# Kernel tuning notes

Measured on AMD Instinct MI355X. Metric: run time of the kernel, lower is better.

## Reference

```python
import jax, jax.numpy as jnp
import numpy as np

NUM_USERS, NUM_ITEMS = 100000, 50000
N_NODES = NUM_USERS + NUM_ITEMS
N_EDGES = 4_000_000
H = 64
BATCH = 100000
MLP_HIDDEN = 32
N_LAYERS = 3


def setup_inputs() -> dict:
    key = jax.random.key(0)
    ks = jax.random.split(key, 12)
    return {
        "edge_index": jax.random.randint(ks[0], (2, N_EDGES), 0, N_NODES, dtype=jnp.int32),
        "user_ids": jax.random.randint(ks[1], (BATCH,), 0, NUM_USERS, dtype=jnp.int32),
        "item_ids": jax.random.randint(ks[2], (BATCH,), 0, NUM_ITEMS, dtype=jnp.int32),
        "user_emb": jax.random.normal(ks[3], (NUM_USERS, H), jnp.float32),
        "item_emb": jax.random.normal(ks[4], (NUM_ITEMS, H), jnp.float32),
        "Wl": jax.random.normal(ks[5], (N_LAYERS, H, H), jnp.float32) * (1.0 / jnp.sqrt(H)),
        "bl": jnp.zeros((N_LAYERS, H), jnp.float32),
        "Wr": jax.random.normal(ks[6], (N_LAYERS, H, H), jnp.float32) * (1.0 / jnp.sqrt(H)),
        "W1": jax.random.normal(ks[7], (2 * H, MLP_HIDDEN), jnp.float32) * (1.0 / jnp.sqrt(2.0 * H)),
        "b1": jnp.zeros((MLP_HIDDEN,), jnp.float32),
        "W2": jax.random.normal(ks[8], (MLP_HIDDEN, 1), jnp.float32) * (1.0 / jnp.sqrt(1.0 * MLP_HIDDEN)),
        "b2": jnp.zeros((1,), jnp.float32),
    }


def _sage_layer(x, src, dst, Wl_i, bl_i, Wr_i):
    # PyG SAGEConv, mean aggr: out = lin_l(mean_{j in N(i)} x_j) + lin_r(x_i)
    msg = x[src]                                                  # [E, H] gather
    summed = jax.ops.segment_sum(msg, dst, num_segments=N_NODES)  # [N, H] scatter-add
    cnt = jax.ops.segment_sum(jnp.ones((src.shape[0],), x.dtype), dst, num_segments=N_NODES)
    mean = summed / jnp.maximum(cnt, 1.0)[:, None]                # empty neighborhoods -> 0
    return mean @ Wl_i + bl_i + x @ Wr_i


def reference(edge_index, user_ids, item_ids, user_emb, item_emb, Wl, bl, Wr, W1, b1, W2, b2):
    src, dst = edge_index[0], edge_index[1]
    x = jnp.concatenate([user_emb, item_emb], axis=0)  # [N, H]
    for l in range(N_LAYERS):
        x = jax.nn.relu(_sage_layer(x, src, dst, Wl[l], bl[l], Wr[l]))
        # dropout is identity in eval mode
    ue = x[user_ids]                   # [B, H]
    ie = x[item_ids + NUM_USERS]       # [B, H]
    pair = jnp.concatenate([ue, ie], axis=-1)  # [B, 2H]
    h = jax.nn.relu(pair @ W1 + b1)
    rating = (h @ W2 + b2)[:, 0]
    return jnp.clip(rating, 1.0, 5.0)
```

## Files before the change

### kernel.cpp

```cpp
#include <hip/hip_runtime.h>
#include <hip/hip_bf16.h>

#define NUM_USERS 100000
#define NUM_ITEMS 50000
#define N_NODES   150000
#define N_EDGES   4000000
#define H         64
#define BATCH     100000
#define MLP_HIDDEN 32
#define NBUCK     586
#define BCAP      8192

typedef unsigned short ushort_t;

__device__ __forceinline__ float bf2f(ushort_t u) {
    return __uint_as_float(((unsigned)u) << 16);
}
__device__ __forceinline__ ushort_t f2bf(float f) {
    unsigned u = __float_as_uint(f);
    u = u + 0x7FFFu + ((u >> 16) & 1u);
    return (ushort_t)(u >> 16);
}
__device__ __forceinline__ float bfLO(unsigned u) { return __uint_as_float(u << 16); }
__device__ __forceinline__ float bfHI(unsigned u) { return __uint_as_float(u & 0xFFFF0000u); }

__global__ __launch_bounds__(256) void init_kernel(const float* __restrict__ ue,
                                                   const float* __restrict__ ie,
                                                   float* __restrict__ x,
                                                   ushort_t* __restrict__ xh) {
    int i = blockIdx.x * 256 + threadIdx.x;
    const int UN4 = NUM_USERS * H / 4;
    float4 v = (i < UN4) ? ((const float4*)ue)[i] : ((const float4*)ie)[i - UN4];
    ((float4*)x)[i] = v;
    uint2 p;
    p.x = (unsigned)f2bf(v.x) | ((unsigned)f2bf(v.y) << 16);
    p.y = (unsigned)f2bf(v.z) | ((unsigned)f2bf(v.w) << 16);
    ((uint2*)xh)[i] = p;
}

#define SCHUNK 2048
__global__ __launch_bounds__(256) void bucket_scatter_kernel(const int* __restrict__ src,
                                                             const int* __restrict__ dst,
                                                             int* __restrict__ bucketCnt,
                                                             int* __restrict__ ebuf) {
    __shared__ int histL[NBUCK];
    __shared__ int curL[NBUCK];
    int base = blockIdx.x * SCHUNK;
    int end = min(base + SCHUNK, N_EDGES);
    for (int i = threadIdx.x; i < NBUCK; i += 256) histL[i] = 0;
    __syncthreads();
    for (int e = base + threadIdx.x; e < end; e += 256)
        atomicAdd(&histL[dst[e] >> 8], 1);
    __syncthreads();
    for (int b = threadIdx.x; b < NBUCK; b += 256)
        curL[b] = histL[b] ? (b * BCAP + atomicAdd(&bucketCnt[b], histL[b])) : 0;
    __syncthreads();
    for (int e = base + threadIdx.x; e < end; e += 256) {
        int d = dst[e];
        int pos = atomicAdd(&curL[d >> 8], 1);
        ebuf[pos] = (src[e] << 8) | (d & 255);
    }
}

__global__ __launch_bounds__(512) void bucket_build_kernel(const int* __restrict__ ebuf,
                                                           const int* __restrict__ bucketCnt,
                                                           int* __restrict__ deg,
                                                           int* __restrict__ offsets,
                                                           int* __restrict__ csr) {
    __shared__ int degL[256];
    __shared__ int scanL[256];
    __shared__ int curL[256];
    int t = threadIdx.x;
    int b = blockIdx.x;
    int nodeBase = b << 8;
    int start = b * BCAP;
    int cnt = bucketCnt[b];

    if (t < 256) degL[t] = 0;
    __syncthreads();
    for (int i = t; i < cnt; i += 512)
        atomicAdd(&degL[ebuf[start + i] & 255], 1);
    __syncthreads();

    int v = (t < 256) ? degL[t] : 0;
    if (t < 256) scanL[t] = v;
    __syncthreads();
#pragma unroll
    for (int off = 1; off < 256; off <<= 1) {
        int u = (t >= off && t < 256) ? scanL[t - off] : 0;
        __syncthreads();
        if (t < 256) scanL[t] += u;
        __syncthreads();
    }

    if (t < 256) {
        int excl = scanL[t] - v;
        int node = nodeBase + t;
        if (node < N_NODES) {
            deg[node] = v;
            offsets[node] = start + excl;
        }
        curL[t] = excl;
    }
    __syncthreads();

    for (int i = t; i < cnt; i += 512) {
        unsigned p = (unsigned)ebuf[start + i];
        int pos = atomicAdd(&curL[p & 255u], 1);
        csr[start + pos] = (int)(p >> 8);
    }
}

__global__ __launch_bounds__(256, 8) void gather_mean_kernel(const ushort_t* __restrict__ xh,
                                                             ushort_t* __restrict__ mean_bf,
                                                             const int* __restrict__ offsets,
                                                             const int* __restrict__ deg,
                                                             const int* __restrict__ csr) {
    int slot = threadIdx.x >> 6;
    int lane = threadIdx.x & 63;
    int q    = lane >> 4;
    int fp   = lane & 15;
    int node = blockIdx.x * 4 + slot;

    int base = offsets[node];
    int cnt  = deg[node];
    const uint2* xr = (const uint2*)xh;

    float a0 = 0.f, a1 = 0.f, a2 = 0.f, a3 = 0.f;

    for (int c = 0; c < cnt; c += 64) {
        int n = min(64, cnt - c);
        int sid = (c + lane < cnt) ? csr[base + c + lane] : 0;
        int nquad = (n + 3) >> 2;
#define PROC(JJ) { int e = 4 * (JJ) + q;                                  \
        int s = __shfl(sid, e, 64);                                       \
        uint2 u = xr[s * 16 + fp];                                        \
        if (c + e >= cnt) { u.x = 0u; u.y = 0u; }                         \
        a0 += bfLO(u.x); a1 += bfHI(u.x); a2 += bfLO(u.y); a3 += bfHI(u.y); }
        int j = 0;
        for (; j + 2 <= nquad; j += 2) { PROC(j) PROC(j + 1) }
        for (; j < nquad; ++j) { PROC(j) }
#undef PROC
    }

    a0 += __shfl_xor(a0, 16, 64); a1 += __shfl_xor(a1, 16, 64);
    a2 += __shfl_xor(a2, 16, 64); a3 += __shfl_xor(a3, 16, 64);
    a0 += __shfl_xor(a0, 32, 64); a1 += __shfl_xor(a1, 32, 64);
    a2 += __shfl_xor(a2, 32, 64); a3 += __shfl_xor(a3, 32, 64);

    if (lane < 16) {
        float rc = 1.0f / fmaxf((float)cnt, 1.0f);
        uint2 p;
        p.x = (unsigned)f2bf(a0 * rc) | ((unsigned)f2bf(a1 * rc) << 16);
        p.y = (unsigned)f2bf(a2 * rc) | ((unsigned)f2bf(a3 * rc) << 16);
        *(uint2*)&mean_bf[node * H + fp * 4] = p;
    }
}

__global__ __launch_bounds__(256) void transform_kernel(float* __restrict__ x,
                                                        ushort_t* __restrict__ xh,
                                                        const ushort_t* __restrict__ mean_bf,
                                                        const float* __restrict__ Wl,
                                                        const float* __restrict__ bl,
                                                        const float* __restrict__ Wr,
                                                        int writeBf) {
    __shared__ float    sWl[H * H];
    __shared__ float    sWr[H * H];
    __shared__ unsigned sMT[H / 2][128];
    __shared__ unsigned sXT[H / 2][128];

    int t = threadIdx.x;
    int node0 = blockIdx.x * 128;

    for (int i = t; i < H * H / 4; i += 256) {
        ((float4*)sWl)[i] = ((const float4*)Wl)[i];
        ((float4*)sWr)[i] = ((const float4*)Wr)[i];
    }
#pragma unroll
    for (int it = 0; it < 8; ++it) {
        int idx = it * 256 + t;
        int n = idx & 127;
        int qd = idx >> 7;
        int node = node0 + n;
        uint2 mu = make_uint2(0u, 0u);
        uint2 xu = make_uint2(0u, 0u);
        if (node < N_NODES) {
            mu = *(const uint2*)&mean_bf[node * H + qd * 4];
            float4 xv = *(const float4*)&x[node * H + qd * 4];
            xu.x = (unsigned)f2bf(xv.x) | ((unsigned)f2bf(xv.y) << 16);
            xu.y = (unsigned)f2bf(xv.z) | ((unsigned)f2bf(xv.w) << 16);
        }
        sMT[qd * 2][n]     = mu.x;
        sMT[qd * 2 + 1][n] = mu.y;
        sXT[qd * 2][n]     = xu.x;
        sXT[qd * 2 + 1][n] = xu.y;
    }
    __syncthreads();

    int tx = t & 7;
    int ty = t >> 3;
    int nbase = node0 + ty * 4;

    float acc[4][8];
#pragma unroll
    for (int j = 0; j < 4; ++j)
#pragma unroll
        for (int f = 0; f < 8; ++f) acc[j][f] = 0.0f;

    for (int kp = 0; kp < H / 2; ++kp) {
        uint4 mu = *(const uint4*)&sMT[kp][ty * 4];
        uint4 xu = *(const uint4*)&sXT[kp][ty * 4];
        int k0 = kp * 2;
        float4 wl00 = *(const float4*)&sWl[k0 * H + tx * 8];
        float4 wl01 = *(const float4*)&sWl[k0 * H + tx * 8 + 4];
        float4 wr00 = *(const float4*)&sWr[k0 * H + tx * 8];
        float4 wr01 = *(const float4*)&sWr[k0 * H + tx * 8 + 4];
        float4 wl10 = *(const float4*)&sWl[(k0 + 1) * H + tx * 8];
        float4 wl11 = *(const float4*)&sWl[(k0 + 1) * H + tx * 8 + 4];
        float4 wr10 = *(const float4*)&sWr[(k0 + 1) * H + tx * 8];
        float4 wr11 = *(const float4*)&sWr[(k0 + 1) * H + tx * 8 + 4];
        const float wl0[8] = {wl00.x, wl00.y, wl00.z, wl00.w, wl01.x, wl01.y, wl01.z, wl01.w};
        const float wr0[8] = {wr00.x, wr00.y, wr00.z, wr00.w, wr01.x, wr01.y, wr01.z, wr01.w};
        const float wl1[8] = {wl10.x, wl10.y, wl10.z, wl10.w, wl11.x, wl11.y, wl11.z, wl11.w};
        const float wr1[8] = {wr10.x, wr10.y, wr10.z, wr10.w, wr11.x, wr11.y, wr11.z, wr11.w};
        const unsigned mua[4] = {mu.x, mu.y, mu.z, mu.w};
        const unsigned xua[4] = {xu.x, xu.y, xu.z, xu.w};
#pragma unroll
        for (int j = 0; j < 4; ++j) {
            float m0 = bfLO(mua[j]), m1 = bfHI(mua[j]);
            float x0 = bfLO(xua[j]), x1 = bfHI(xua[j]);
#pragma unroll
            for (int f = 0; f < 8; ++f) {
                float a = acc[j][f];
                a = fmaf(m0, wl0[f], a);
                a = fmaf(x0, wr0[f], a);
                a = fmaf(m1, wl1[f], a);
                a = fmaf(x1, wr1[f], a);
                acc[j][f] = a;
            }
        }
    }

    float4 b0 = *(const float4*)&bl[tx * 8];
    float4 b1 = *(const float4*)&bl[tx * 8 + 4];
    const float bias[8] = {b0.x, b0.y, b0.z, b0.w, b1.x, b1.y, b1.z, b1.w};
#pragma unroll
    for (int j = 0; j < 4; ++j) {
        int node = nbase + j;
        if (node < N_NODES) {
            float o[8];
#pragma unroll
            for (int f = 0; f < 8; ++f) o[f] = fmaxf(acc[j][f] + bias[f], 0.0f);
            *(float4*)&x[node * H + tx * 8]     = make_float4(o[0], o[1], o[2], o[3]);
            *(float4*)&x[node * H + tx * 8 + 4] = make_float4(o[4], o[5], o[6], o[7]);
            if (writeBf) {
                uint4 p;
                p.x = (unsigned)f2bf(o[0]) | ((unsigned)f2bf(o[1]) << 16);
                p.y = (unsigned)f2bf(o[2]) | ((unsigned)f2bf(o[3]) << 16);
                p.z = (unsigned)f2bf(o[4]) | ((unsigned)f2bf(o[5]) << 16);
                p.w = (unsigned)f2bf(o[6]) | ((unsigned)f2bf(o[7]) << 16);
                *(uint4*)&xh[node * H + tx * 8] = p;
            }
        }
    }
}

__global__ __launch_bounds__(256) void mlp_kernel(const float* __restrict__ x,
                                                  const int* __restrict__ uids,
                                                  const int* __restrict__ iids,
                                                  const float* __restrict__ W1,
                                                  const float* __restrict__ b1,
                                                  const float* __restrict__ W2,
                                                  const float* __restrict__ b2,
                                                  float* __restrict__ out) {
    __shared__ float sW1[2 * H * MLP_HIDDEN];
    __shared__ float sPair[8][2 * H];
    __shared__ float sW2[MLP_HIDDEN];

    for (int i = threadIdx.x; i < 2 * H * MLP_HIDDEN; i += 256) sW1[i] = W1[i];
    if (threadIdx.x < MLP_HIDDEN) sW2[threadIdx.x] = W2[threadIdx.x];

    int slot = threadIdx.x >> 5;
    int j    = threadIdx.x & 31;
    int b = blockIdx.x * 8 + slot;

    int u  = uids[b];
    int it = iids[b] + NUM_USERS;
    float2 a = *(const float2*)&x[u * H + j * 2];
    sPair[slot][j * 2]     = a.x;
    sPair[slot][j * 2 + 1] = a.y;
    float2 c = *(const float2*)&x[it * H + j * 2];
    sPair[slot][H + j * 2]     = c.x;
    sPair[slot][H + j * 2 + 1] = c.y;
    __syncthreads();

    float hacc = b1[j];
#pragma unroll
    for (int k = 0; k < 2 * H; ++k)
        hacc = fmaf(sPair[slot][k], sW1[k * MLP_HIDDEN + j], hacc);
    hacc = fmaxf(hacc, 0.0f);

    float r = hacc * sW2[j];
#pragma unroll
    for (int off = 16; off; off >>= 1) r += __shfl_down(r, off, 32);

    if (j == 0) out[b] = fminf(fmaxf(r + b2[0], 1.0f), 5.0f);
}

extern "C" void kernel_launch(void* const* d_in, const int* in_sizes, int n_in,
                              void* d_out, int out_size, void* d_ws, size_t ws_size,
                              hipStream_t stream) {
    const int*   edge_index = (const int*)d_in[0];
    const int*   user_ids   = (const int*)d_in[1];
    const int*   item_ids   = (const int*)d_in[2];
    const float* user_emb   = (const float*)d_in[3];
    const float* item_emb   = (const float*)d_in[4];
    const float* Wl         = (const float*)d_in[5];
    const float* bl         = (const float*)d_in[6];
    const float* Wr         = (const float*)d_in[7];
    const float* W1         = (const float*)d_in[8];
    const float* b1         = (const float*)d_in[9];
    const float* W2         = (const float*)d_in[10];
    const float* b2         = (const float*)d_in[11];
    float* out = (float*)d_out;

    const int* src = edge_index;
    const int* dst = edge_index + N_EDGES;

    const size_t NH = (size_t)N_NODES * H;
    float* x          = (float*)d_ws;
    int* ebuf         = (int*)(x + NH);
    ushort_t* mean_bf = (ushort_t*)ebuf;
    ushort_t* xh      = (ushort_t*)(ebuf + (size_t)NBUCK * BCAP);
    int* deg          = (int*)(xh + NH);
    int* offsets      = deg + N_NODES;
    int* bucketCnt    = offsets + N_NODES;
    int* csr          = bucketCnt + NBUCK;

    init_kernel<<<(N_NODES * H / 4) / 256, 256, 0, stream>>>(user_emb, item_emb, x, xh);

    hipMemsetAsync(bucketCnt, 0, NBUCK * sizeof(int), stream);
    bucket_scatter_kernel<<<(N_EDGES + SCHUNK - 1) / SCHUNK, 256, 0, stream>>>(
        src, dst, bucketCnt, ebuf);
    bucket_build_kernel<<<NBUCK, 512, 0, stream>>>(ebuf, bucketCnt, deg, offsets, csr);

    const int TGRID = (N_NODES + 127) / 128;
    for (int l = 0; l < 3; ++l) {
        gather_mean_kernel<<<N_NODES / 4, 256, 0, stream>>>(xh, mean_bf, offsets, deg, csr);
        transform_kernel<<<TGRID, 256, 0, stream>>>(
            x, xh, mean_bf, Wl + (size_t)l * H * H, bl + (size_t)l * H,
            Wr + (size_t)l * H * H, l < 2 ? 1 : 0);
    }

    mlp_kernel<<<BATCH / 8, 256, 0, stream>>>(x, user_ids, item_ids, W1, b1, W2, b2, out);
}
```

Before: 561.1 us.

## Stage bucket scatter in LDS for coalesced global writes, double chunk size

The edge bucketing kernel now keeps a block's edges in registers, computes a per-block prefix scan of bucket counts, and sorts edges into shared memory by bucket. The global write to ebuf then happens in contiguous runs per bucket, not as random per-edge scattered stores. The chunk size per block is doubled, which halves the number of global bucket-count atomics but adds LDS usage (about 30KB), which may lower occupancy.

```diff
diff --git a/kernel.cpp b/kernel.cpp
--- a/kernel.cpp
+++ b/kernel.cpp
@@ -38,27 +38,80 @@
     ((uint2*)xh)[i] = p;
 }
 
-#define SCHUNK 2048
+#define SCHUNK 4096
+#define SPT    (SCHUNK / 256)
 __global__ __launch_bounds__(256) void bucket_scatter_kernel(const int* __restrict__ src,
                                                              const int* __restrict__ dst,
                                                              int* __restrict__ bucketCnt,
                                                              int* __restrict__ ebuf) {
-    __shared__ int histL[NBUCK];
-    __shared__ int curL[NBUCK];
+    __shared__ int      histL[NBUCK];
+    __shared__ int      startL[NBUCK];
+    __shared__ int      adjL[NBUCK];
+    __shared__ int      curL[NBUCK];
+    __shared__ unsigned staged[SCHUNK];
+    __shared__ ushort_t sbuck[SCHUNK];
+
+    int t = threadIdx.x;
     int base = blockIdx.x * SCHUNK;
-    int end = min(base + SCHUNK, N_EDGES);
-    for (int i = threadIdx.x; i < NBUCK; i += 256) histL[i] = 0;
-    __syncthreads();
-    for (int e = base + threadIdx.x; e < end; e += 256)
-        atomicAdd(&histL[dst[e] >> 8], 1);
-    __syncthreads();
-    for (int b = threadIdx.x; b < NBUCK; b += 256)
-        curL[b] = histL[b] ? (b * BCAP + atomicAdd(&bucketCnt[b], histL[b])) : 0;
-    __syncthreads();
-    for (int e = base + threadIdx.x; e < end; e += 256) {
-        int d = dst[e];
-        int pos = atomicAdd(&curL[d >> 8], 1);
-        ebuf[pos] = (src[e] << 8) | (d & 255);
+    int nst = min(SCHUNK, N_EDGES - base);
+
+    for (int i = t; i < NBUCK; i += 256) histL[i] = 0;
+    __syncthreads();
+
+    int myd[SPT], mys[SPT];
+#pragma unroll
+    for (int k = 0; k < SPT; ++k) {
+        int e = base + k * 256 + t;
+        int d = (e < N_EDGES) ? dst[e] : -1;
+        mys[k] = (e < N_EDGES) ? src[e] : 0;
+        myd[k] = d;
+        if (d >= 0) atomicAdd(&histL[d >> 8], 1);
+    }
+    __syncthreads();
+
+    if (t < 64) {
+        const int CH = (NBUCK + 63) / 64;
+        int s0 = t * CH;
+        int s1 = min(s0 + CH, NBUCK);
+        int s = 0;
+        for (int i = s0; i < s1; ++i) s += histL[i];
+        int v = s;
+#pragma unroll
+        for (int off = 1; off < 64; off <<= 1) {
+            int u = __shfl_up(v, off, 64);
+            if (t >= off) v += u;
+        }
+        int run = v - s;
+        for (int i = s0; i < s1; ++i) {
+            startL[i] = run;
+            run += histL[i];
+        }
+    }
+    __syncthreads();
+
+    for (int b = t; b < NBUCK; b += 256) {
+        int h = histL[b];
+        int res = h ? (b * BCAP + atomicAdd(&bucketCnt[b], h)) : 0;
+        adjL[b] = res - startL[b];
+        curL[b] = startL[b];
+    }
+    __syncthreads();
+
+#pragma unroll
+    for (int k = 0; k < SPT; ++k) {
+        int d = myd[k];
+        if (d >= 0) {
+            int b = d >> 8;
+            int pos = atomicAdd(&curL[b], 1);
+            staged[pos] = ((unsigned)mys[k] << 8) | (unsigned)(d & 255);
+            sbuck[pos] = (ushort_t)b;
+        }
+    }
+    __syncthreads();
+
+    for (int i = t; i < nst; i += 256) {
+        int b = sbuck[i];
+        ebuf[adjL[b] + i] = (int)staged[i];
     }
 }
 
```

Result: faster. 501.4 us (-10.6%).
